# Optimization experiments

Hardware: AMD Instinct MI355X
Metric: run time of the kernel (lower is better)

Reference implementation:

```python
import jax, jax.numpy as jnp
import numpy as np

N0, E0 = 20000, 100000
N1, E1 = 100000, 400000
N2, E2 = 400000, 800000
D = 128
LN_EPS = 1e-5


def gconv(h, src, dst, n, W, b):
    """DGL GraphConv, norm='both', on graph (src,dst) with self-loops added."""
    loops = jnp.arange(n, dtype=src.dtype)
    s = jnp.concatenate([src, loops])
    d = jnp.concatenate([dst, loops])
    ones = jnp.ones(s.shape[0], h.dtype)
    deg_out = jax.ops.segment_sum(ones, s, num_segments=n)
    deg_in = jax.ops.segment_sum(ones, d, num_segments=n)
    hn = (h * jax.lax.rsqrt(jnp.maximum(deg_out, 1.0))[:, None]) @ W
    agg = jax.ops.segment_sum(hn[s], d, num_segments=n)
    return agg * jax.lax.rsqrt(jnp.maximum(deg_in, 1.0))[:, None] + b


def lgcore(src, dst, n, curr_h, fus_inputs, p):
    """fus_inputs: list of (fusion_input [n,D] (already inc-matmul'd), scale [D])."""
    convW, convb, fusW, fusb, catW, catb, convw, lng, lnb = p
    cs = gconv(curr_h, src, dst, n, convW, convb) * convw[None, :]
    res = jnp.concatenate([jax.nn.relu(cs), cs], axis=1)
    for fin, sw in fus_inputs:
        fs = gconv(fin, src, dst, n, fusW, fusb) * sw[None, :]
        res = res + jnp.concatenate([jax.nn.relu(fs), fs], axis=1)
    out = res @ catW + catb
    mu = jnp.mean(out, axis=-1, keepdims=True)
    var = jnp.var(out, axis=-1, keepdims=True)
    return (out - mu) * jax.lax.rsqrt(var + LN_EPS) * lng + lnb


def lgnn(h0, h1, h2, src0, dst0, src1, dst1, src2, dst2,
         convW, convb, fusW, fusb, catW, catb, convw, tdw, buw, lng, lnb):
    def params(i):
        return (convW[i], convb[i], fusW[i], fusb[i], catW[i], catb[i], convw[i], lng[i], lnb[i])
    # level 0: top_down core (idx 0). inc0 @ h1 -> segment_sum of h1 over dst0
    td0 = jax.ops.segment_sum(h1, dst0, num_segments=N0)
    out0 = lgcore(src0, dst0, N0, h0, [(td0, tdw[0])], params(0))
    # level 1: 'both' core (idx 2). inc0^T @ h0 -> gather; inc1 @ h2 -> segment_sum
    bu1 = h0[dst0]                                   # [E0=N1, D]
    td1 = jax.ops.segment_sum(h2, dst1, num_segments=N1)
    out1 = lgcore(src1, dst1, N1, h1, [(bu1, buw[2]), (td1, tdw[2])], params(2))
    # level 2: bottom_up core (idx 1). inc1^T @ h1 -> gather
    bu2 = h1[dst1]                                   # [E1=N2, D]
    out2 = lgcore(src2, dst2, N2, h2, [(bu2, buw[1])], params(1))
    return out0, out1, out2


def setup_inputs() -> dict:
    key = jax.random.key(0)
    ks = jax.random.split(key, 16)
    sc = 1.0 / np.sqrt(D)
    return {
        "h0": jax.random.normal(ks[0], (N0, D), jnp.float32),
        "h1": jax.random.normal(ks[1], (N1, D), jnp.float32),
        "h2": jax.random.normal(ks[2], (N2, D), jnp.float32),
        "src0": jax.random.randint(ks[3], (E0,), 0, N0, jnp.int32),
        "dst0": jax.random.randint(ks[4], (E0,), 0, N0, jnp.int32),
        "src1": jax.random.randint(ks[5], (E1,), 0, N1, jnp.int32),
        "dst1": jax.random.randint(ks[6], (E1,), 0, N1, jnp.int32),
        "src2": jax.random.randint(ks[7], (E2,), 0, N2, jnp.int32),
        "dst2": jax.random.randint(ks[8], (E2,), 0, N2, jnp.int32),
        "convW": jax.random.normal(ks[9], (3, D, D), jnp.float32) * sc,
        "convb": jnp.zeros((3, D), jnp.float32),
        "fusW": jax.random.normal(ks[10], (3, D, D), jnp.float32) * sc,
        "fusb": jnp.zeros((3, D), jnp.float32),
        "catW": jax.random.normal(ks[11], (3, 2 * D, D), jnp.float32) * (1.0 / np.sqrt(2 * D)),
        "catb": jnp.zeros((3, D), jnp.float32),
        "convw": jax.random.uniform(ks[12], (3, D), jnp.float32),
        "tdw": jax.random.uniform(ks[13], (3, D), jnp.float32),
        "buw": jax.random.uniform(ks[14], (3, D), jnp.float32),
        "lng": jnp.ones((3, D), jnp.float32),
        "lnb": jnp.zeros((3, D), jnp.float32),
    }


def reference(h0, h1, h2, src0, dst0, src1, dst1, src2, dst2,
              convW, convb, fusW, fusb, catW, catb, convw, tdw, buw, lng, lnb):
    return lgnn(h0, h1, h2, src0, dst0, src1, dst1, src2, dst2,
                convW, convb, fusW, fusb, catW, catb, convw, tdw, buw, lng, lnb)
```

## Files before the change

### kernel.cpp

```cpp
#include <hip/hip_runtime.h>

#define D 128
#define LN_EPS 1e-5f

static constexpr int cN0 = 20000,  cE0 = 100000;
static constexpr int cN1 = 100000, cE1 = 400000;
static constexpr int cN2 = 400000, cE2 = 800000;

typedef _Float16 f16;
typedef _Float16 f16x8 __attribute__((ext_vector_type(8)));
typedef float f32x4 __attribute__((ext_vector_type(4)));
typedef unsigned short u16x8 __attribute__((ext_vector_type(8)));

__device__ inline float h2f(unsigned short u) {
    return (float)__builtin_bit_cast(_Float16, u);
}
__device__ inline unsigned short f2h(float f) {
    return __builtin_bit_cast(unsigned short, (_Float16)f);
}
__device__ inline float4 h4_to_f4(ushort4 v) {
    return make_float4(h2f(v.x), h2f(v.y), h2f(v.z), h2f(v.w));
}


__global__ void k_count(const int* __restrict__ src, const int* __restrict__ dst,
                        int* cnt_out, int* cnt_in, int E) {
    int e = blockIdx.x * blockDim.x + threadIdx.x;
    if (e < E) {
        atomicAdd(&cnt_out[src[e]], 1);
        atomicAdd(&cnt_in[dst[e]], 1);
    }
}

__global__ void k_bsum(const int* __restrict__ cnt, int* bsum, int n) {
    __shared__ int sd[256];
    int t = threadIdx.x;
    int base = blockIdx.x * 1024 + t * 4;
    int s = 0;
#pragma unroll
    for (int i = 0; i < 4; ++i) { int idx = base + i; if (idx < n) s += cnt[idx]; }
    sd[t] = s; __syncthreads();
    for (int off = 128; off > 0; off >>= 1) {
        if (t < off) sd[t] += sd[t + off];
        __syncthreads();
    }
    if (t == 0) bsum[blockIdx.x] = sd[0];
}

__global__ void k_scan_write(const int* __restrict__ cnt, const int* __restrict__ bsum,
                             int* __restrict__ ptr, int n, int E) {
    __shared__ int sd[256];
    __shared__ int so[256];
    int t = threadIdx.x, blk = blockIdx.x;
    int off = 0;
    for (int i = t; i < blk; i += 256) off += bsum[i];
    so[t] = off; __syncthreads();
    for (int o = 128; o > 0; o >>= 1) { if (t < o) so[t] += so[t + o]; __syncthreads(); }
    int boff = so[0];
    int base = blk * 1024 + t * 4;
    int vals[4]; int s = 0;
#pragma unroll
    for (int i = 0; i < 4; ++i) { int idx = base + i; vals[i] = (idx < n) ? cnt[idx] : 0; s += vals[i]; }
    sd[t] = s; __syncthreads();
    for (int o = 1; o < 256; o <<= 1) {
        int x = (t >= o) ? sd[t - o] : 0;
        __syncthreads();
        sd[t] += x;
        __syncthreads();
    }
    int run = boff + sd[t] - s;
#pragma unroll
    for (int i = 0; i < 4; ++i) {
        int idx = base + i;
        if (idx < n) ptr[idx] = run;
        run += vals[i];
    }
    if (blk == 0 && t == 0) ptr[n] = E;
}

__global__ void k_rin_cursor(const int* __restrict__ cnt_out, const int* __restrict__ cnt_in,
                             const int* __restrict__ ptr, float* __restrict__ rout,
                             float* __restrict__ rin, int* __restrict__ cursor, int n) {
    int i = blockIdx.x * blockDim.x + threadIdx.x;
    if (i < n) {
        rout[i] = rsqrtf((float)(cnt_out[i] + 1));
        rin[i]  = rsqrtf((float)(cnt_in[i] + 1));
        cursor[i] = ptr[i];
    }
}

__global__ void k_fill(const int* __restrict__ src, const int* __restrict__ dst,
                       int* cursor, int* __restrict__ eid, int* __restrict__ srcs, int E) {
    int e = blockIdx.x * blockDim.x + threadIdx.x;
    if (e < E) {
        int p = atomicAdd(&cursor[dst[e]], 1);
        eid[p] = e;
        srcs[p] = src[e];
    }
}

__global__ void k_segsum_rows(float* __restrict__ X, const int* __restrict__ ptr,
                              const int* __restrict__ eid, const float* __restrict__ table,
                              int n) {
    int wid = (blockIdx.x * blockDim.x + threadIdx.x) >> 6;
    int lane = threadIdx.x & 63;
    if (wid >= n) return;
    int j = lane * 2;
    float2 acc = make_float2(0.f, 0.f);
    int p0 = ptr[wid], p1 = ptr[wid + 1];
    for (int p = p0; p < p1; ++p) {
        int e = eid[p];
        const float2 x = *(const float2*)(table + (size_t)e * D + j);
        acc.x += x.x; acc.y += x.y;
    }
    *(float2*)(X + (size_t)wid * D + j) = acc;
}

__global__ void k_prep_w(const float* __restrict__ convW, const float* __restrict__ fusW,
                         const float* __restrict__ catW,
                         unsigned short* __restrict__ cWt, unsigned short* __restrict__ fWt,
                         unsigned short* __restrict__ kWt) {
    int t = blockIdx.x * 256 + threadIdx.x;
    if (t < 98304) {
        int mi = t / 16384, r = t % 16384;
        const float* W = (mi < 3) ? (convW + mi * 16384) : (fusW + (mi - 3) * 16384);
        unsigned short* T = (mi < 3) ? (cWt + mi * 16384) : (fWt + (mi - 3) * 16384);
        int n = r >> 7, k = r & 127;
        T[r] = f2h(W[k * 128 + n]);
    } else if (t < 196608) {
        int t2 = t - 98304;
        int mi = t2 / 32768, r = t2 % 32768;
        int n = r >> 8, k = r & 255;
        kWt[mi * 32768 + r] = f2h(catW[mi * 32768 + k * 128 + n]);
    }
}

template<bool GATHER>
__global__ __launch_bounds__(256) void k_gconv_mfma(
        const float* __restrict__ A, const int* __restrict__ ridx,
        const float* __restrict__ rs, const unsigned short* __restrict__ Wt,
        unsigned short* __restrict__ C, int M) {
    __shared__ __align__(16) unsigned short Ws[128 * 128];
    int tid = threadIdx.x;
#pragma unroll
    for (int i = 0; i < 8; ++i) {
        int lb = (tid + i * 256) << 4;
        int n = lb >> 8;
        int sw = lb ^ ((n & 7) << 4);
        *(u16x8*)((char*)Ws + sw) = *(const u16x8*)((const char*)Wt + lb);
    }
    __syncthreads();
    int w = tid >> 6, l = tid & 63;
    int g = l >> 4, ln = l & 15;
    int row0 = blockIdx.x * 128 + w * 32;
    int m0 = row0 + ln, m1 = m0 + 16;
    bool v0 = m0 < M, v1 = m1 < M;
    int sr0 = m0, sr1 = m1;
    if (GATHER) {
        sr0 = v0 ? ridx[m0] : 0;
        sr1 = v1 ? ridx[m1] : 0;
    }
    const float* a0p = A + (size_t)sr0 * 128;
    const float* a1p = A + (size_t)sr1 * 128;
    f32x4 acc[2][8] = {};
#pragma unroll
    for (int k0 = 0; k0 < 128; k0 += 32) {
        int kk = k0 + g * 8;
        f16x8 b0 = {}, b1 = {};
        if (v0) {
            float4 x = *(const float4*)(a0p + kk);
            float4 y = *(const float4*)(a0p + kk + 4);
            b0[0] = (f16)x.x; b0[1] = (f16)x.y; b0[2] = (f16)x.z; b0[3] = (f16)x.w;
            b0[4] = (f16)y.x; b0[5] = (f16)y.y; b0[6] = (f16)y.z; b0[7] = (f16)y.w;
        }
        if (v1) {
            float4 x = *(const float4*)(a1p + kk);
            float4 y = *(const float4*)(a1p + kk + 4);
            b1[0] = (f16)x.x; b1[1] = (f16)x.y; b1[2] = (f16)x.z; b1[3] = (f16)x.w;
            b1[4] = (f16)y.x; b1[5] = (f16)y.y; b1[6] = (f16)y.z; b1[7] = (f16)y.w;
        }
#pragma unroll
        for (int nf = 0; nf < 8; ++nf) {
            int n = nf * 16 + ln;
            int sw = (n * 256 + kk * 2) ^ ((n & 7) << 4);
            f16x8 a = *(const f16x8*)((const char*)Ws + sw);
            acc[0][nf] = __builtin_amdgcn_mfma_f32_16x16x32_f16(a, b0, acc[0][nf], 0, 0, 0);
            acc[1][nf] = __builtin_amdgcn_mfma_f32_16x16x32_f16(a, b1, acc[1][nf], 0, 0, 0);
        }
    }
    float s0 = v0 ? rs[m0] : 0.f;
    float s1 = v1 ? rs[m1] : 0.f;
#pragma unroll
    for (int mf = 0; mf < 2; ++mf) {
        int m = mf ? m1 : m0;
        if (m >= M) continue;
        float s = mf ? s1 : s0;
        unsigned short* cp = C + (size_t)m * 128 + g * 4;
#pragma unroll
        for (int nf = 0; nf < 8; ++nf) {
            f32x4 v = acc[mf][nf];
            ushort4 o;
            o.x = f2h(v[0] * s); o.y = f2h(v[1] * s);
            o.z = f2h(v[2] * s); o.w = f2h(v[3] * s);
            *(ushort4*)(cp + nf * 16) = o;
        }
    }
}

template<int NT>
__global__ void k_agg_multi(const unsigned short* __restrict__ H0,
                            const unsigned short* __restrict__ H1,
                            const unsigned short* __restrict__ H2,
                            const int* __restrict__ ptr, const int* __restrict__ srcs,
                            const float* __restrict__ rin,
                            const float* __restrict__ b0, const float* __restrict__ b1,
                            const float* __restrict__ b2,
                            const float* __restrict__ c0, const float* __restrict__ c1,
                            const float* __restrict__ c2,
                            unsigned short* __restrict__ RES, int n) {
    int node = (blockIdx.x * blockDim.x + threadIdx.x) >> 5;
    int lane = threadIdx.x & 31;
    if (node >= n) return;
    int j = lane * 4;

    float4 a0 = make_float4(0.f, 0.f, 0.f, 0.f), a1 = a0, a2 = a0;
    a0 = h4_to_f4(*(const ushort4*)(H0 + (size_t)node * D + j));
    if (NT > 1) a1 = h4_to_f4(*(const ushort4*)(H1 + (size_t)node * D + j));
    if (NT > 2) a2 = h4_to_f4(*(const ushort4*)(H2 + (size_t)node * D + j));

    int p0 = ptr[node], p1 = ptr[node + 1];
    for (int p = p0; p < p1; ++p) {
        int s = srcs[p];
        float4 x0 = h4_to_f4(*(const ushort4*)(H0 + (size_t)s * D + j));
        a0.x += x0.x; a0.y += x0.y; a0.z += x0.z; a0.w += x0.w;
        if (NT > 1) {
            float4 x1 = h4_to_f4(*(const ushort4*)(H1 + (size_t)s * D + j));
            a1.x += x1.x; a1.y += x1.y; a1.z += x1.z; a1.w += x1.w;
        }
        if (NT > 2) {
            float4 x2 = h4_to_f4(*(const ushort4*)(H2 + (size_t)s * D + j));
            a2.x += x2.x; a2.y += x2.y; a2.z += x2.z; a2.w += x2.w;
        }
    }

    float ri = rin[node];
    float4 bb0 = *(const float4*)(b0 + j);
    float4 cc0 = *(const float4*)(c0 + j);
    float4 v, rsum, ssum;
    v.x = (a0.x * ri + bb0.x) * cc0.x;
    v.y = (a0.y * ri + bb0.y) * cc0.y;
    v.z = (a0.z * ri + bb0.z) * cc0.z;
    v.w = (a0.w * ri + bb0.w) * cc0.w;
    rsum = make_float4(fmaxf(v.x, 0.f), fmaxf(v.y, 0.f), fmaxf(v.z, 0.f), fmaxf(v.w, 0.f));
    ssum = v;
    if (NT > 1) {
        float4 bb = *(const float4*)(b1 + j);
        float4 cc = *(const float4*)(c1 + j);
        v.x = (a1.x * ri + bb.x) * cc.x;
        v.y = (a1.y * ri + bb.y) * cc.y;
        v.z = (a1.z * ri + bb.z) * cc.z;
        v.w = (a1.w * ri + bb.w) * cc.w;
        rsum.x += fmaxf(v.x, 0.f); rsum.y += fmaxf(v.y, 0.f);
        rsum.z += fmaxf(v.z, 0.f); rsum.w += fmaxf(v.w, 0.f);
        ssum.x += v.x; ssum.y += v.y; ssum.z += v.z; ssum.w += v.w;
    }
    if (NT > 2) {
        float4 bb = *(const float4*)(b2 + j);
        float4 cc = *(const float4*)(c2 + j);
        v.x = (a2.x * ri + bb.x) * cc.x;
        v.y = (a2.y * ri + bb.y) * cc.y;
        v.z = (a2.z * ri + bb.z) * cc.z;
        v.w = (a2.w * ri + bb.w) * cc.w;
        rsum.x += fmaxf(v.x, 0.f); rsum.y += fmaxf(v.y, 0.f);
        rsum.z += fmaxf(v.z, 0.f); rsum.w += fmaxf(v.w, 0.f);
        ssum.x += v.x; ssum.y += v.y; ssum.z += v.z; ssum.w += v.w;
    }
    unsigned short* r = RES + (size_t)node * (2 * D) + j;
    ushort4 o1, o2;
    o1.x = f2h(rsum.x); o1.y = f2h(rsum.y); o1.z = f2h(rsum.z); o1.w = f2h(rsum.w);
    o2.x = f2h(ssum.x); o2.y = f2h(ssum.y); o2.z = f2h(ssum.z); o2.w = f2h(ssum.w);
    *(ushort4*)r = o1;
    *(ushort4*)(r + D) = o2;
}

__global__ __launch_bounds__(256) void k_cat_ln_mfma(
        const unsigned short* __restrict__ RESh, const unsigned short* __restrict__ Wt,
        const float* __restrict__ bias, const float* __restrict__ gam,
        const float* __restrict__ bet, float* __restrict__ out, int M) {
    __shared__ __align__(16) unsigned short Ws[128 * 256];
    int tid = threadIdx.x;
#pragma unroll
    for (int i = 0; i < 16; ++i) {
        int lb = (tid + i * 256) << 4;
        int n = lb >> 9;
        int sw = lb ^ ((n & 7) << 4);
        *(u16x8*)((char*)Ws + sw) = *(const u16x8*)((const char*)Wt + lb);
    }
    __syncthreads();
    int w = tid >> 6, l = tid & 63;
    int g = l >> 4, ln = l & 15;
    int row0 = blockIdx.x * 128 + w * 32;
    int m0 = row0 + ln, m1 = m0 + 16;
    bool v0 = m0 < M, v1 = m1 < M;
    const unsigned short* r0p = RESh + (size_t)m0 * 256;
    const unsigned short* r1p = RESh + (size_t)m1 * 256;
    f32x4 acc[2][8] = {};
#pragma unroll
    for (int k0 = 0; k0 < 256; k0 += 32) {
        int kk = k0 + g * 8;
        f16x8 b0 = {}, b1 = {};
        if (v0) b0 = *(const f16x8*)(r0p + kk);
        if (v1) b1 = *(const f16x8*)(r1p + kk);
#pragma unroll
        for (int nf = 0; nf < 8; ++nf) {
            int n = nf * 16 + ln;
            int sw = (n * 512 + kk * 2) ^ ((n & 7) << 4);
            f16x8 a = *(const f16x8*)((const char*)Ws + sw);
            acc[0][nf] = __builtin_amdgcn_mfma_f32_16x16x32_f16(a, b0, acc[0][nf], 0, 0, 0);
            acc[1][nf] = __builtin_amdgcn_mfma_f32_16x16x32_f16(a, b1, acc[1][nf], 0, 0, 0);
        }
    }
#pragma unroll
    for (int mf = 0; mf < 2; ++mf) {
        float x[8][4];
        float s = 0.f, ss = 0.f;
#pragma unroll
        for (int nf = 0; nf < 8; ++nf) {
            float4 b = *(const float4*)(bias + nf * 16 + g * 4);
            f32x4 v = acc[mf][nf];
            x[nf][0] = v[0] + b.x; x[nf][1] = v[1] + b.y;
            x[nf][2] = v[2] + b.z; x[nf][3] = v[3] + b.w;
            s += x[nf][0] + x[nf][1] + x[nf][2] + x[nf][3];
            ss += x[nf][0] * x[nf][0] + x[nf][1] * x[nf][1]
                + x[nf][2] * x[nf][2] + x[nf][3] * x[nf][3];
        }
        s  += __shfl_xor(s, 16, 64);  s  += __shfl_xor(s, 32, 64);
        ss += __shfl_xor(ss, 16, 64); ss += __shfl_xor(ss, 32, 64);
        float mu = s * (1.0f / 128.0f);
        float var = ss * (1.0f / 128.0f) - mu * mu;
        float inv = rsqrtf(var + LN_EPS);
        int m = mf ? m1 : m0;
        if (m < M) {
            float* op = out + (size_t)m * 128 + g * 4;
#pragma unroll
            for (int nf = 0; nf < 8; ++nf) {
                float4 gv = *(const float4*)(gam + nf * 16 + g * 4);
                float4 ev = *(const float4*)(bet + nf * 16 + g * 4);
                float4 o;
                o.x = (x[nf][0] - mu) * inv * gv.x + ev.x;
                o.y = (x[nf][1] - mu) * inv * gv.y + ev.y;
                o.z = (x[nf][2] - mu) * inv * gv.z + ev.z;
                o.w = (x[nf][3] - mu) * inv * gv.w + ev.w;
                *(float4*)(op + nf * 16) = o;
            }
        }
    }
}

__global__ void k_ws_too_small(float* out) {
    if (threadIdx.x == 0 && blockIdx.x == 0) out[0] = 12345678.f;
}


struct Lvl {
    int n, E;
    const int *src, *dst;
    int *cnt_out, *cnt_in, *ptr, *cursor, *eid, *srcs;
    float *rout, *rin;
};

static inline char* bump(char*& p, size_t bytes, void** out) {
    *out = (void*)p;
    p += (bytes + 255) & ~(size_t)255;
    return p;
}

extern "C" void kernel_launch(void* const* d_in, const int* in_sizes, int n_in,
                              void* d_out, int out_size, void* d_ws, size_t ws_size,
                              hipStream_t stream) {
    const float* h0 = (const float*)d_in[0];
    const float* h1 = (const float*)d_in[1];
    const float* h2 = (const float*)d_in[2];
    const int* src0 = (const int*)d_in[3];
    const int* dst0 = (const int*)d_in[4];
    const int* src1 = (const int*)d_in[5];
    const int* dst1 = (const int*)d_in[6];
    const int* src2 = (const int*)d_in[7];
    const int* dst2 = (const int*)d_in[8];
    const float* convW = (const float*)d_in[9];
    const float* convb = (const float*)d_in[10];
    const float* fusW  = (const float*)d_in[11];
    const float* fusb  = (const float*)d_in[12];
    const float* catW  = (const float*)d_in[13];
    const float* catb  = (const float*)d_in[14];
    const float* convw = (const float*)d_in[15];
    const float* tdw   = (const float*)d_in[16];
    const float* buw   = (const float*)d_in[17];
    const float* lng   = (const float*)d_in[18];
    const float* lnb   = (const float*)d_in[19];
    float* out = (float*)d_out;

    char* p = (char*)d_ws;
    void *vX, *vHNa, *vHNb, *vHNc, *vRES, *vbsum, *vcWt, *vfWt, *vkWt;
    bump(p, (size_t)cN1 * D * 4, &vX);
    bump(p, (size_t)cN2 * D * 2, &vHNa);
    bump(p, (size_t)cN2 * D * 2, &vHNb);
    bump(p, (size_t)cN1 * D * 2, &vHNc);
    bump(p, (size_t)cN2 * 2 * D * 2, &vRES);
    bump(p, 512 * 4, &vbsum);
    bump(p, (size_t)3 * 128 * 128 * 2, &vcWt);
    bump(p, (size_t)3 * 128 * 128 * 2, &vfWt);
    bump(p, (size_t)3 * 128 * 256 * 2, &vkWt);
    float* X = (float*)vX;
    unsigned short* HNa = (unsigned short*)vHNa;
    unsigned short* HNb = (unsigned short*)vHNb;
    unsigned short* HNc = (unsigned short*)vHNc;
    unsigned short* RESh = (unsigned short*)vRES;
    int* bsum = (int*)vbsum;
    unsigned short* cWt = (unsigned short*)vcWt;
    unsigned short* fWt = (unsigned short*)vfWt;
    unsigned short* kWt = (unsigned short*)vkWt;

    Lvl lv[3];
    lv[0] = {cN0, cE0, src0, dst0};
    lv[1] = {cN1, cE1, src1, dst1};
    lv[2] = {cN2, cE2, src2, dst2};
    for (int L = 0; L < 3; ++L) {
        Lvl& v = lv[L];
        void* t;
        bump(p, (size_t)v.n * 4, &t);       v.cnt_out = (int*)t;
        bump(p, (size_t)v.n * 4, &t);       v.cnt_in  = (int*)t;
        bump(p, (size_t)(v.n + 1) * 4, &t); v.ptr     = (int*)t;
        bump(p, (size_t)v.n * 4, &t);       v.cursor  = (int*)t;
        bump(p, (size_t)v.E * 4, &t);       v.eid     = (int*)t;
        bump(p, (size_t)v.E * 4, &t);       v.srcs    = (int*)t;
        bump(p, (size_t)v.n * 4, &t);       v.rout    = (float*)t;
        bump(p, (size_t)v.n * 4, &t);       v.rin     = (float*)t;
    }
    size_t need = (size_t)(p - (char*)d_ws);
    if (need > ws_size) {
        hipLaunchKernelGGL(k_ws_too_small, dim3(1), dim3(64), 0, stream, out);
        return;
    }

    k_prep_w<<<768, 256, 0, stream>>>(convW, fusW, catW, cWt, fWt, kWt);

    for (int L = 0; L < 3; ++L) {
        Lvl& v = lv[L];
        hipMemsetAsync(v.cnt_out, 0, (size_t)v.n * 4, stream);
        hipMemsetAsync(v.cnt_in, 0, (size_t)v.n * 4, stream);
        k_count<<<(v.E + 255) / 256, 256, 0, stream>>>(v.src, v.dst, v.cnt_out, v.cnt_in, v.E);
        int nb = (v.n + 1023) / 1024;
        k_bsum<<<nb, 256, 0, stream>>>(v.cnt_in, bsum, v.n);
        k_scan_write<<<nb, 256, 0, stream>>>(v.cnt_in, bsum, v.ptr, v.n, v.E);
        k_rin_cursor<<<(v.n + 255) / 256, 256, 0, stream>>>(v.cnt_out, v.cnt_in, v.ptr,
                                                            v.rout, v.rin, v.cursor, v.n);
        k_fill<<<(v.E + 255) / 256, 256, 0, stream>>>(v.src, v.dst, v.cursor, v.eid, v.srcs, v.E);
    }

    auto gemm = [&](int L, const float* A, const int* ridx, const unsigned short* Wt,
                    unsigned short* HN) {
        Lvl& v = lv[L];
        int nb = (v.n + 127) / 128;
        if (ridx)
            k_gconv_mfma<true><<<nb, 256, 0, stream>>>(A, ridx, v.rout, Wt, HN, v.n);
        else
            k_gconv_mfma<false><<<nb, 256, 0, stream>>>(A, nullptr, v.rout, Wt, HN, v.n);
    };

    {
        Lvl& v = lv[0];
        gemm(0, h0, nullptr, cWt, HNa);
        k_segsum_rows<<<(cN0 + 3) / 4, 256, 0, stream>>>(X, v.ptr, v.eid, h1, cN0);
        gemm(0, X, nullptr, fWt, HNb);
        k_agg_multi<2><<<(cN0 * 32 + 255) / 256, 256, 0, stream>>>(
            HNa, HNb, HNa, v.ptr, v.srcs, v.rin,
            convb + 0, fusb + 0, convb + 0,
            convw + 0, tdw + 0, convw + 0, RESh, cN0);
        k_cat_ln_mfma<<<(cN0 + 127) / 128, 256, 0, stream>>>(RESh, kWt, catb + 0,
                                                             lng + 0, lnb + 0, out, cN0);
    }

    {
        Lvl& v = lv[1];
        const int o1 = 2 * D;
        gemm(1, h1, nullptr, cWt + 2 * 16384, HNa);
        gemm(1, h0, dst0, fWt + 2 * 16384, HNb);
        k_segsum_rows<<<(cN1 + 3) / 4, 256, 0, stream>>>(X, v.ptr, v.eid, h2, cN1);
        gemm(1, X, nullptr, fWt + 2 * 16384, HNc);
        k_agg_multi<3><<<(cN1 * 32 + 255) / 256, 256, 0, stream>>>(
            HNa, HNb, HNc, v.ptr, v.srcs, v.rin,
            convb + o1, fusb + o1, fusb + o1,
            convw + o1, buw + o1, tdw + o1, RESh, cN1);
        k_cat_ln_mfma<<<(cN1 + 127) / 128, 256, 0, stream>>>(RESh, kWt + 2 * 32768, catb + o1,
                                                             lng + o1, lnb + o1,
                                                             out + (size_t)cN0 * D, cN1);
    }

    {
        Lvl& v = lv[2];
        const int o1 = 1 * D;
        gemm(2, h2, nullptr, cWt + 1 * 16384, HNa);
        gemm(2, h1, dst1, fWt + 1 * 16384, HNb);
        k_agg_multi<2><<<(cN2 * 32 + 255) / 256, 256, 0, stream>>>(
            HNa, HNb, HNa, v.ptr, v.srcs, v.rin,
            convb + o1, fusb + o1, convb + o1,
            convw + o1, buw + o1, convw + o1, RESh, cN2);
        k_cat_ln_mfma<<<(cN2 + 127) / 128, 256, 0, stream>>>(RESh, kWt + 1 * 32768, catb + o1,
                                                             lng + o1, lnb + o1,
                                                             out + (size_t)(cN0 + cN1) * D, cN2);
    }
}
```

Before: 1.334 ms.

## Aggregate before projecting and fuse per-source GEMMs with concat-LN

Reorders each graph convolution as aggregate-then-multiply, using linearity of the weight matmul. It gathers fp16 inputs (converted once up front) scaled by out-degree, then runs a single fused kernel that does all per-source 128x128 MFMA GEMMs, applies bias and scale, relu and sum, the concat GEMM and the LayerNorm. This removes the HN intermediate buffers and the RES round trip through global memory, and folds the per-feature scales into the weights. The cost is that weights are read from global/L1 inside the MFMA loop rather than staged in LDS, and inputs plus segment sums are now held in fp16, which adds rounding error.

```diff
diff --git a/kernel.cpp b/kernel.cpp
--- a/kernel.cpp
+++ b/kernel.cpp
@@ -17,9 +17,6 @@
 }
 __device__ inline unsigned short f2h(float f) {
     return __builtin_bit_cast(unsigned short, (_Float16)f);
-}
-__device__ inline float4 h4_to_f4(ushort4 v) {
-    return make_float4(h2f(v.x), h2f(v.y), h2f(v.z), h2f(v.w));
 }
 
 
@@ -99,260 +96,272 @@
     }
 }
 
-__global__ void k_segsum_rows(float* __restrict__ X, const int* __restrict__ ptr,
-                              const int* __restrict__ eid, const float* __restrict__ table,
-                              int n) {
+__global__ void k_f2h(const float* __restrict__ in, unsigned short* __restrict__ o, int n4) {
+    int i = blockIdx.x * 256 + threadIdx.x;
+    if (i < n4) {
+        float4 v = ((const float4*)in)[i];
+        ushort4 u;
+        u.x = f2h(v.x); u.y = f2h(v.y); u.z = f2h(v.z); u.w = f2h(v.w);
+        ((ushort4*)o)[i] = u;
+    }
+}
+
+__global__ void k_segsum_h(unsigned short* __restrict__ X, const int* __restrict__ ptr,
+                           const int* __restrict__ eid, const unsigned short* __restrict__ table,
+                           int n) {
     int wid = (blockIdx.x * blockDim.x + threadIdx.x) >> 6;
     int lane = threadIdx.x & 63;
     if (wid >= n) return;
     int j = lane * 2;
-    float2 acc = make_float2(0.f, 0.f);
+    float ax = 0.f, ay = 0.f;
     int p0 = ptr[wid], p1 = ptr[wid + 1];
     for (int p = p0; p < p1; ++p) {
         int e = eid[p];
-        const float2 x = *(const float2*)(table + (size_t)e * D + j);
-        acc.x += x.x; acc.y += x.y;
-    }
-    *(float2*)(X + (size_t)wid * D + j) = acc;
+        ushort2 u = *(const ushort2*)(table + (size_t)e * D + j);
+        ax += h2f(u.x); ay += h2f(u.y);
+    }
+    ushort2 o; o.x = f2h(ax); o.y = f2h(ay);
+    *(ushort2*)(X + (size_t)wid * D + j) = o;
 }
 
 __global__ void k_prep_w(const float* __restrict__ convW, const float* __restrict__ fusW,
                          const float* __restrict__ catW,
-                         unsigned short* __restrict__ cWt, unsigned short* __restrict__ fWt,
-                         unsigned short* __restrict__ kWt) {
+                         const float* __restrict__ convw, const float* __restrict__ tdw,
+                         const float* __restrict__ buw,
+                         unsigned short* __restrict__ sWt, unsigned short* __restrict__ kWt) {
     int t = blockIdx.x * 256 + threadIdx.x;
-    if (t < 98304) {
-        int mi = t / 16384, r = t % 16384;
-        const float* W = (mi < 3) ? (convW + mi * 16384) : (fusW + (mi - 3) * 16384);
-        unsigned short* T = (mi < 3) ? (cWt + mi * 16384) : (fWt + (mi - 3) * 16384);
+    if (t < 7 * 16384) {
+        int slot = t / 16384, r = t % 16384;
         int n = r >> 7, k = r & 127;
-        T[r] = f2h(W[k * 128 + n]);
-    } else if (t < 196608) {
-        int t2 = t - 98304;
-        int mi = t2 / 32768, r = t2 % 32768;
-        int n = r >> 8, k = r & 255;
-        kWt[mi * 32768 + r] = f2h(catW[mi * 32768 + k * 128 + n]);
-    }
-}
-
-template<bool GATHER>
-__global__ __launch_bounds__(256) void k_gconv_mfma(
-        const float* __restrict__ A, const int* __restrict__ ridx,
-        const float* __restrict__ rs, const unsigned short* __restrict__ Wt,
-        unsigned short* __restrict__ C, int M) {
-    __shared__ __align__(16) unsigned short Ws[128 * 128];
-    int tid = threadIdx.x;
-#pragma unroll
-    for (int i = 0; i < 8; ++i) {
-        int lb = (tid + i * 256) << 4;
-        int n = lb >> 8;
-        int sw = lb ^ ((n & 7) << 4);
-        *(u16x8*)((char*)Ws + sw) = *(const u16x8*)((const char*)Wt + lb);
-    }
-    __syncthreads();
-    int w = tid >> 6, l = tid & 63;
-    int g = l >> 4, ln = l & 15;
-    int row0 = blockIdx.x * 128 + w * 32;
-    int m0 = row0 + ln, m1 = m0 + 16;
-    bool v0 = m0 < M, v1 = m1 < M;
-    int sr0 = m0, sr1 = m1;
-    if (GATHER) {
-        sr0 = v0 ? ridx[m0] : 0;
-        sr1 = v1 ? ridx[m1] : 0;
-    }
-    const float* a0p = A + (size_t)sr0 * 128;
-    const float* a1p = A + (size_t)sr1 * 128;
-    f32x4 acc[2][8] = {};
-#pragma unroll
-    for (int k0 = 0; k0 < 128; k0 += 32) {
-        int kk = k0 + g * 8;
-        f16x8 b0 = {}, b1 = {};
-        if (v0) {
-            float4 x = *(const float4*)(a0p + kk);
-            float4 y = *(const float4*)(a0p + kk + 4);
-            b0[0] = (f16)x.x; b0[1] = (f16)x.y; b0[2] = (f16)x.z; b0[3] = (f16)x.w;
-            b0[4] = (f16)y.x; b0[5] = (f16)y.y; b0[6] = (f16)y.z; b0[7] = (f16)y.w;
-        }
-        if (v1) {
-            float4 x = *(const float4*)(a1p + kk);
-            float4 y = *(const float4*)(a1p + kk + 4);
-            b1[0] = (f16)x.x; b1[1] = (f16)x.y; b1[2] = (f16)x.z; b1[3] = (f16)x.w;
-            b1[4] = (f16)y.x; b1[5] = (f16)y.y; b1[6] = (f16)y.z; b1[7] = (f16)y.w;
-        }
-#pragma unroll
-        for (int nf = 0; nf < 8; ++nf) {
-            int n = nf * 16 + ln;
-            int sw = (n * 256 + kk * 2) ^ ((n & 7) << 4);
-            f16x8 a = *(const f16x8*)((const char*)Ws + sw);
-            acc[0][nf] = __builtin_amdgcn_mfma_f32_16x16x32_f16(a, b0, acc[0][nf], 0, 0, 0);
-            acc[1][nf] = __builtin_amdgcn_mfma_f32_16x16x32_f16(a, b1, acc[1][nf], 0, 0, 0);
-        }
-    }
-    float s0 = v0 ? rs[m0] : 0.f;
-    float s1 = v1 ? rs[m1] : 0.f;
-#pragma unroll
-    for (int mf = 0; mf < 2; ++mf) {
-        int m = mf ? m1 : m0;
-        if (m >= M) continue;
-        float s = mf ? s1 : s0;
-        unsigned short* cp = C + (size_t)m * 128 + g * 4;
-#pragma unroll
-        for (int nf = 0; nf < 8; ++nf) {
-            f32x4 v = acc[mf][nf];
-            ushort4 o;
-            o.x = f2h(v[0] * s); o.y = f2h(v[1] * s);
-            o.z = f2h(v[2] * s); o.w = f2h(v[3] * s);
-            *(ushort4*)(cp + nf * 16) = o;
-        }
-    }
-}
-
-template<int NT>
-__global__ void k_agg_multi(const unsigned short* __restrict__ H0,
-                            const unsigned short* __restrict__ H1,
-                            const unsigned short* __restrict__ H2,
-                            const int* __restrict__ ptr, const int* __restrict__ srcs,
-                            const float* __restrict__ rin,
-                            const float* __restrict__ b0, const float* __restrict__ b1,
-                            const float* __restrict__ b2,
-                            const float* __restrict__ c0, const float* __restrict__ c1,
-                            const float* __restrict__ c2,
-                            unsigned short* __restrict__ RES, int n) {
+        const float* W; const float* cw;
+        switch (slot) {
+            case 0: W = convW;              cw = convw;            break;
+            case 1: W = fusW;               cw = tdw;              break;
+            case 2: W = convW + 2 * 16384;  cw = convw + 2 * 128;  break;
+            case 3: W = fusW + 2 * 16384;   cw = buw + 2 * 128;    break;
+            case 4: W = fusW + 2 * 16384;   cw = tdw + 2 * 128;    break;
+            case 5: W = convW + 1 * 16384;  cw = convw + 1 * 128;  break;
+            default: W = fusW + 1 * 16384;  cw = buw + 1 * 128;    break;
+        }
+        sWt[t] = f2h(W[k * 128 + n] * cw[n]);
+    } else {
+        int t2 = t - 7 * 16384;
+        if (t2 < 3 * 32768) {
+            int mi = t2 / 32768, r = t2 % 32768;
+            int n = r >> 8, k = r & 255;
+            kWt[mi * 32768 + r] = f2h(catW[mi * 32768 + k * 128 + n]);
+        }
+    }
+}
+
+template<int NT, bool G1>
+__global__ void k_aggh(const unsigned short* __restrict__ F0,
+                       const unsigned short* __restrict__ F1,
+                       const unsigned short* __restrict__ F2,
+                       const int* __restrict__ gidx,
+                       const float* __restrict__ rout,
+                       const int* __restrict__ ptr, const int* __restrict__ srcs,
+                       unsigned short* __restrict__ A0, unsigned short* __restrict__ A1,
+                       unsigned short* __restrict__ A2, int n) {
     int node = (blockIdx.x * blockDim.x + threadIdx.x) >> 5;
     int lane = threadIdx.x & 31;
     if (node >= n) return;
     int j = lane * 4;
 
-    float4 a0 = make_float4(0.f, 0.f, 0.f, 0.f), a1 = a0, a2 = a0;
-    a0 = h4_to_f4(*(const ushort4*)(H0 + (size_t)node * D + j));
-    if (NT > 1) a1 = h4_to_f4(*(const ushort4*)(H1 + (size_t)node * D + j));
-    if (NT > 2) a2 = h4_to_f4(*(const ushort4*)(H2 + (size_t)node * D + j));
+    float rt = rout[node];
+    float4 a0, a1, a2;
+    {
+        ushort4 u = *(const ushort4*)(F0 + (size_t)node * D + j);
+        a0 = make_float4(h2f(u.x) * rt, h2f(u.y) * rt, h2f(u.z) * rt, h2f(u.w) * rt);
+    }
+    if (NT > 1) {
+        int i1 = G1 ? gidx[node] : node;
+        ushort4 u = *(const ushort4*)(F1 + (size_t)i1 * D + j);
+        a1 = make_float4(h2f(u.x) * rt, h2f(u.y) * rt, h2f(u.z) * rt, h2f(u.w) * rt);
+    }
+    if (NT > 2) {
+        ushort4 u = *(const ushort4*)(F2 + (size_t)node * D + j);
+        a2 = make_float4(h2f(u.x) * rt, h2f(u.y) * rt, h2f(u.z) * rt, h2f(u.w) * rt);
+    }
 
     int p0 = ptr[node], p1 = ptr[node + 1];
-    for (int p = p0; p < p1; ++p) {
-        int s = srcs[p];
-        float4 x0 = h4_to_f4(*(const ushort4*)(H0 + (size_t)s * D + j));
-        a0.x += x0.x; a0.y += x0.y; a0.z += x0.z; a0.w += x0.w;
+    int p = p0;
+    for (; p + 2 <= p1; p += 2) {
+        int sA = srcs[p], sB = srcs[p + 1];
+        float rA = rout[sA], rB = rout[sB];
+        ushort4 uA = *(const ushort4*)(F0 + (size_t)sA * D + j);
+        ushort4 uB = *(const ushort4*)(F0 + (size_t)sB * D + j);
+        a0.x += h2f(uA.x) * rA + h2f(uB.x) * rB;
+        a0.y += h2f(uA.y) * rA + h2f(uB.y) * rB;
+        a0.z += h2f(uA.z) * rA + h2f(uB.z) * rB;
+        a0.w += h2f(uA.w) * rA + h2f(uB.w) * rB;
         if (NT > 1) {
-            float4 x1 = h4_to_f4(*(const ushort4*)(H1 + (size_t)s * D + j));
-            a1.x += x1.x; a1.y += x1.y; a1.z += x1.z; a1.w += x1.w;
+            int iA = G1 ? gidx[sA] : sA;
+            int iB = G1 ? gidx[sB] : sB;
+            ushort4 vA = *(const ushort4*)(F1 + (size_t)iA * D + j);
+            ushort4 vB = *(const ushort4*)(F1 + (size_t)iB * D + j);
+            a1.x += h2f(vA.x) * rA + h2f(vB.x) * rB;
+            a1.y += h2f(vA.y) * rA + h2f(vB.y) * rB;
+            a1.z += h2f(vA.z) * rA + h2f(vB.z) * rB;
+            a1.w += h2f(vA.w) * rA + h2f(vB.w) * rB;
         }
         if (NT > 2) {
-            float4 x2 = h4_to_f4(*(const ushort4*)(H2 + (size_t)s * D + j));
-            a2.x += x2.x; a2.y += x2.y; a2.z += x2.z; a2.w += x2.w;
-        }
-    }
-
-    float ri = rin[node];
-    float4 bb0 = *(const float4*)(b0 + j);
-    float4 cc0 = *(const float4*)(c0 + j);
-    float4 v, rsum, ssum;
-    v.x = (a0.x * ri + bb0.x) * cc0.x;
-    v.y = (a0.y * ri + bb0.y) * cc0.y;
-    v.z = (a0.z * ri + bb0.z) * cc0.z;
-    v.w = (a0.w * ri + bb0.w) * cc0.w;
-    rsum = make_float4(fmaxf(v.x, 0.f), fmaxf(v.y, 0.f), fmaxf(v.z, 0.f), fmaxf(v.w, 0.f));
-    ssum = v;
+            ushort4 vA = *(const ushort4*)(F2 + (size_t)sA * D + j);
+            ushort4 vB = *(const ushort4*)(F2 + (size_t)sB * D + j);
+            a2.x += h2f(vA.x) * rA + h2f(vB.x) * rB;
+            a2.y += h2f(vA.y) * rA + h2f(vB.y) * rB;
+            a2.z += h2f(vA.z) * rA + h2f(vB.z) * rB;
+            a2.w += h2f(vA.w) * rA + h2f(vB.w) * rB;
+        }
+    }
+    if (p < p1) {
+        int sA = srcs[p];
+        float rA = rout[sA];
+        ushort4 uA = *(const ushort4*)(F0 + (size_t)sA * D + j);
+        a0.x += h2f(uA.x) * rA; a0.y += h2f(uA.y) * rA;
+        a0.z += h2f(uA.z) * rA; a0.w += h2f(uA.w) * rA;
+        if (NT > 1) {
+            int iA = G1 ? gidx[sA] : sA;
+            ushort4 vA = *(const ushort4*)(F1 + (size_t)iA * D + j);
+            a1.x += h2f(vA.x) * rA; a1.y += h2f(vA.y) * rA;
+            a1.z += h2f(vA.z) * rA; a1.w += h2f(vA.w) * rA;
+        }
+        if (NT > 2) {
+            ushort4 vA = *(const ushort4*)(F2 + (size_t)sA * D + j);
+            a2.x += h2f(vA.x) * rA; a2.y += h2f(vA.y) * rA;
+            a2.z += h2f(vA.z) * rA; a2.w += h2f(vA.w) * rA;
+        }
+    }
+
+    ushort4 o;
+    o.x = f2h(a0.x); o.y = f2h(a0.y); o.z = f2h(a0.z); o.w = f2h(a0.w);
+    *(ushort4*)(A0 + (size_t)node * D + j) = o;
     if (NT > 1) {
-        float4 bb = *(const float4*)(b1 + j);
-        float4 cc = *(const float4*)(c1 + j);
-        v.x = (a1.x * ri + bb.x) * cc.x;
-        v.y = (a1.y * ri + bb.y) * cc.y;
-        v.z = (a1.z * ri + bb.z) * cc.z;
-        v.w = (a1.w * ri + bb.w) * cc.w;
-        rsum.x += fmaxf(v.x, 0.f); rsum.y += fmaxf(v.y, 0.f);
-        rsum.z += fmaxf(v.z, 0.f); rsum.w += fmaxf(v.w, 0.f);
-        ssum.x += v.x; ssum.y += v.y; ssum.z += v.z; ssum.w += v.w;
+        o.x = f2h(a1.x); o.y = f2h(a1.y); o.z = f2h(a1.z); o.w = f2h(a1.w);
+        *(ushort4*)(A1 + (size_t)node * D + j) = o;
     }
     if (NT > 2) {
-        float4 bb = *(const float4*)(b2 + j);
-        float4 cc = *(const float4*)(c2 + j);
-        v.x = (a2.x * ri + bb.x) * cc.x;
-        v.y = (a2.y * ri + bb.y) * cc.y;
-        v.z = (a2.z * ri + bb.z) * cc.z;
-        v.w = (a2.w * ri + bb.w) * cc.w;
-        rsum.x += fmaxf(v.x, 0.f); rsum.y += fmaxf(v.y, 0.f);
-        rsum.z += fmaxf(v.z, 0.f); rsum.w += fmaxf(v.w, 0.f);
-        ssum.x += v.x; ssum.y += v.y; ssum.z += v.z; ssum.w += v.w;
-    }
-    unsigned short* r = RES + (size_t)node * (2 * D) + j;
-    ushort4 o1, o2;
-    o1.x = f2h(rsum.x); o1.y = f2h(rsum.y); o1.z = f2h(rsum.z); o1.w = f2h(rsum.w);
-    o2.x = f2h(ssum.x); o2.y = f2h(ssum.y); o2.z = f2h(ssum.z); o2.w = f2h(ssum.w);
-    *(ushort4*)r = o1;
-    *(ushort4*)(r + D) = o2;
-}
-
-__global__ __launch_bounds__(256) void k_cat_ln_mfma(
-        const unsigned short* __restrict__ RESh, const unsigned short* __restrict__ Wt,
-        const float* __restrict__ bias, const float* __restrict__ gam,
-        const float* __restrict__ bet, float* __restrict__ out, int M) {
-    __shared__ __align__(16) unsigned short Ws[128 * 256];
+        o.x = f2h(a2.x); o.y = f2h(a2.y); o.z = f2h(a2.z); o.w = f2h(a2.w);
+        *(ushort4*)(A2 + (size_t)node * D + j) = o;
+    }
+}
+
+template<int NT>
+__global__ __launch_bounds__(256) void k_mega(
+        const unsigned short* __restrict__ A0h, const unsigned short* __restrict__ A1h,
+        const unsigned short* __restrict__ A2h,
+        const unsigned short* __restrict__ W0, const unsigned short* __restrict__ W1,
+        const unsigned short* __restrict__ W2,
+        const float* __restrict__ pb0, const float* __restrict__ pc0,
+        const float* __restrict__ pb1, const float* __restrict__ pc1,
+        const float* __restrict__ pb2, const float* __restrict__ pc2,
+        const float* __restrict__ rin,
+        const unsigned short* __restrict__ kWt,
+        const float* __restrict__ cbias, const float* __restrict__ gam,
+        const float* __restrict__ bet,
+        float* __restrict__ out, int M) {
+    __shared__ __align__(16) unsigned short tile[64 * 256];
     int tid = threadIdx.x;
-#pragma unroll
-    for (int i = 0; i < 16; ++i) {
-        int lb = (tid + i * 256) << 4;
-        int n = lb >> 9;
-        int sw = lb ^ ((n & 7) << 4);
-        *(u16x8*)((char*)Ws + sw) = *(const u16x8*)((const char*)Wt + lb);
+    int w = tid >> 6, l = tid & 63, g = l >> 4, ln = l & 15;
+    int mloc = w * 16 + ln;
+    int m = blockIdx.x * 64 + mloc;
+    bool vm = m < M;
+    float ri = vm ? rin[m] : 0.f;
+
+    f32x4 rr[8] = {};
+    f32x4 sv[8] = {};
+
+    const unsigned short* Ah[3] = {A0h, A1h, A2h};
+    const unsigned short* Wh[3] = {W0, W1, W2};
+    const float* pbs[3] = {pb0, pb1, pb2};
+    const float* pcs[3] = {pc0, pc1, pc2};
+
+#pragma unroll
+    for (int t = 0; t < NT; ++t) {
+        f32x4 acc[8] = {};
+        const unsigned short* ap = Ah[t] + (size_t)m * 128;
+#pragma unroll
+        for (int k0 = 0; k0 < 128; k0 += 32) {
+            int kk = k0 + g * 8;
+            f16x8 bf = {};
+            if (vm) bf = *(const f16x8*)(ap + kk);
+#pragma unroll
+            for (int nf = 0; nf < 8; ++nf) {
+                f16x8 af = *(const f16x8*)(Wh[t] + (size_t)(nf * 16 + ln) * 128 + kk);
+                acc[nf] = __builtin_amdgcn_mfma_f32_16x16x32_f16(af, bf, acc[nf], 0, 0, 0);
+            }
+        }
+#pragma unroll
+        for (int nf = 0; nf < 8; ++nf) {
+            float4 bb = *(const float4*)(pbs[t] + nf * 16 + g * 4);
+            float4 cc = *(const float4*)(pcs[t] + nf * 16 + g * 4);
+            f32x4 a = acc[nf];
+            float v0 = ri * a[0] + bb.x * cc.x;
+            float v1 = ri * a[1] + bb.y * cc.y;
+            float v2 = ri * a[2] + bb.z * cc.z;
+            float v3 = ri * a[3] + bb.w * cc.w;
+            rr[nf][0] += fmaxf(v0, 0.f); rr[nf][1] += fmaxf(v1, 0.f);
+            rr[nf][2] += fmaxf(v2, 0.f); rr[nf][3] += fmaxf(v3, 0.f);
+            sv[nf][0] += v0; sv[nf][1] += v1; sv[nf][2] += v2; sv[nf][3] += v3;
+        }
+    }
+
+#pragma unroll
+    for (int nf = 0; nf < 8; ++nf) {
+        int n = nf * 16 + g * 4;
+        int byr = (mloc * 512 + n * 2) ^ ((mloc & 7) << 4);
+        ushort4 ur, us;
+        ur.x = f2h(rr[nf][0]); ur.y = f2h(rr[nf][1]);
+        ur.z = f2h(rr[nf][2]); ur.w = f2h(rr[nf][3]);
+        us.x = f2h(sv[nf][0]); us.y = f2h(sv[nf][1]);
+        us.z = f2h(sv[nf][2]); us.w = f2h(sv[nf][3]);
+        *(ushort4*)((char*)tile + byr) = ur;
+        *(ushort4*)((char*)tile + byr + 256) = us;
     }
     __syncthreads();
-    int w = tid >> 6, l = tid & 63;
-    int g = l >> 4, ln = l & 15;
-    int row0 = blockIdx.x * 128 + w * 32;
-    int m0 = row0 + ln, m1 = m0 + 16;
-    bool v0 = m0 < M, v1 = m1 < M;
-    const unsigned short* r0p = RESh + (size_t)m0 * 256;
-    const unsigned short* r1p = RESh + (size_t)m1 * 256;
-    f32x4 acc[2][8] = {};
+
+    f32x4 acc2[8] = {};
 #pragma unroll
     for (int k0 = 0; k0 < 256; k0 += 32) {
         int kk = k0 + g * 8;
-        f16x8 b0 = {}, b1 = {};
-        if (v0) b0 = *(const f16x8*)(r0p + kk);
-        if (v1) b1 = *(const f16x8*)(r1p + kk);
+        int by = (mloc * 512 + kk * 2) ^ ((mloc & 7) << 4);
+        f16x8 bf = *(const f16x8*)((const char*)tile + by);
 #pragma unroll
         for (int nf = 0; nf < 8; ++nf) {
-            int n = nf * 16 + ln;
-            int sw = (n * 512 + kk * 2) ^ ((n & 7) << 4);
-            f16x8 a = *(const f16x8*)((const char*)Ws + sw);
-            acc[0][nf] = __builtin_amdgcn_mfma_f32_16x16x32_f16(a, b0, acc[0][nf], 0, 0, 0);
-            acc[1][nf] = __builtin_amdgcn_mfma_f32_16x16x32_f16(a, b1, acc[1][nf], 0, 0, 0);
-        }
-    }
-#pragma unroll
-    for (int mf = 0; mf < 2; ++mf) {
-        float x[8][4];
-        float s = 0.f, ss = 0.f;
+            f16x8 af = *(const f16x8*)(kWt + (size_t)(nf * 16 + ln) * 256 + kk);
+            acc2[nf] = __builtin_amdgcn_mfma_f32_16x16x32_f16(af, bf, acc2[nf], 0, 0, 0);
+        }
+    }
+
+    float x[8][4];
+    float sum = 0.f, ssum = 0.f;
+#pragma unroll
+    for (int nf = 0; nf < 8; ++nf) {
+        float4 b = *(const float4*)(cbias + nf * 16 + g * 4);
+        f32x4 vv = acc2[nf];
+        x[nf][0] = vv[0] + b.x; x[nf][1] = vv[1] + b.y;
+        x[nf][2] = vv[2] + b.z; x[nf][3] = vv[3] + b.w;
+        sum += x[nf][0] + x[nf][1] + x[nf][2] + x[nf][3];
+        ssum += x[nf][0] * x[nf][0] + x[nf][1] * x[nf][1]
+              + x[nf][2] * x[nf][2] + x[nf][3] * x[nf][3];
+    }
+    sum  += __shfl_xor(sum, 16, 64);  sum  += __shfl_xor(sum, 32, 64);
+    ssum += __shfl_xor(ssum, 16, 64); ssum += __shfl_xor(ssum, 32, 64);
+    float mu = sum * (1.0f / 128.0f);
+    float var = ssum * (1.0f / 128.0f) - mu * mu;
+    float inv = rsqrtf(var + LN_EPS);
+    if (vm) {
+        float* op = out + (size_t)m * 128 + g * 4;
 #pragma unroll
         for (int nf = 0; nf < 8; ++nf) {
-            float4 b = *(const float4*)(bias + nf * 16 + g * 4);
-            f32x4 v = acc[mf][nf];
-            x[nf][0] = v[0] + b.x; x[nf][1] = v[1] + b.y;
-            x[nf][2] = v[2] + b.z; x[nf][3] = v[3] + b.w;
-            s += x[nf][0] + x[nf][1] + x[nf][2] + x[nf][3];
-            ss += x[nf][0] * x[nf][0] + x[nf][1] * x[nf][1]
-                + x[nf][2] * x[nf][2] + x[nf][3] * x[nf][3];
-        }
-        s  += __shfl_xor(s, 16, 64);  s  += __shfl_xor(s, 32, 64);
-        ss += __shfl_xor(ss, 16, 64); ss += __shfl_xor(ss, 32, 64);
-        float mu = s * (1.0f / 128.0f);
-        float var = ss * (1.0f / 128.0f) - mu * mu;
-        float inv = rsqrtf(var + LN_EPS);
-        int m = mf ? m1 : m0;
-        if (m < M) {
-            float* op = out + (size_t)m * 128 + g * 4;
-#pragma unroll
-            for (int nf = 0; nf < 8; ++nf) {
-                float4 gv = *(const float4*)(gam + nf * 16 + g * 4);
-                float4 ev = *(const float4*)(bet + nf * 16 + g * 4);
-                float4 o;
-                o.x = (x[nf][0] - mu) * inv * gv.x + ev.x;
-                o.y = (x[nf][1] - mu) * inv * gv.y + ev.y;
-                o.z = (x[nf][2] - mu) * inv * gv.z + ev.z;
-                o.w = (x[nf][3] - mu) * inv * gv.w + ev.w;
-                *(float4*)(op + nf * 16) = o;
-            }
+            float4 gv = *(const float4*)(gam + nf * 16 + g * 4);
+            float4 ev = *(const float4*)(bet + nf * 16 + g * 4);
+            float4 o;
+            o.x = (x[nf][0] - mu) * inv * gv.x + ev.x;
+            o.y = (x[nf][1] - mu) * inv * gv.y + ev.y;
+            o.z = (x[nf][2] - mu) * inv * gv.z + ev.z;
+            o.w = (x[nf][3] - mu) * inv * gv.w + ev.w;
+            *(float4*)(op + nf * 16) = o;
         }
     }
 }
@@ -401,25 +410,27 @@
     float* out = (float*)d_out;
 
     char* p = (char*)d_ws;
-    void *vX, *vHNa, *vHNb, *vHNc, *vRES, *vbsum, *vcWt, *vfWt, *vkWt;
-    bump(p, (size_t)cN1 * D * 4, &vX);
-    bump(p, (size_t)cN2 * D * 2, &vHNa);
-    bump(p, (size_t)cN2 * D * 2, &vHNb);
-    bump(p, (size_t)cN1 * D * 2, &vHNc);
-    bump(p, (size_t)cN2 * 2 * D * 2, &vRES);
+    void *vh0f, *vh1f, *vh2f, *vXf, *vAa, *vAb, *vAc, *vsWt, *vkWt, *vbsum;
+    bump(p, (size_t)cN0 * D * 2, &vh0f);
+    bump(p, (size_t)cN1 * D * 2, &vh1f);
+    bump(p, (size_t)cN2 * D * 2, &vh2f);
+    bump(p, (size_t)cN1 * D * 2, &vXf);
+    bump(p, (size_t)cN2 * D * 2, &vAa);
+    bump(p, (size_t)cN2 * D * 2, &vAb);
+    bump(p, (size_t)cN1 * D * 2, &vAc);
+    bump(p, (size_t)7 * 16384 * 2, &vsWt);
+    bump(p, (size_t)3 * 32768 * 2, &vkWt);
     bump(p, 512 * 4, &vbsum);
-    bump(p, (size_t)3 * 128 * 128 * 2, &vcWt);
-    bump(p, (size_t)3 * 128 * 128 * 2, &vfWt);
-    bump(p, (size_t)3 * 128 * 256 * 2, &vkWt);
-    float* X = (float*)vX;
-    unsigned short* HNa = (unsigned short*)vHNa;
-    unsigned short* HNb = (unsigned short*)vHNb;
-    unsigned short* HNc = (unsigned short*)vHNc;
-    unsigned short* RESh = (unsigned short*)vRES;
+    unsigned short* h0f = (unsigned short*)vh0f;
+    unsigned short* h1f = (unsigned short*)vh1f;
+    unsigned short* h2f = (unsigned short*)vh2f;
+    unsigned short* Xf  = (unsigned short*)vXf;
+    unsigned short* Aa  = (unsigned short*)vAa;
+    unsigned short* Ab  = (unsigned short*)vAb;
+    unsigned short* Ac  = (unsigned short*)vAc;
+    unsigned short* sWt = (unsigned short*)vsWt;
+    unsigned short* kWt = (unsigned short*)vkWt;
     int* bsum = (int*)vbsum;
-    unsigned short* cWt = (unsigned short*)vcWt;
-    unsigned short* fWt = (unsigned short*)vfWt;
-    unsigned short* kWt = (unsigned short*)vkWt;
 
     Lvl lv[3];
     lv[0] = {cN0, cE0, src0, dst0};
@@ -443,7 +454,10 @@
         return;
     }
 
-    k_prep_w<<<768, 256, 0, stream>>>(convW, fusW, catW, cWt, fWt, kWt);
+    k_prep_w<<<832, 256, 0, stream>>>(convW, fusW, catW, convw, tdw, buw, sWt, kWt);
+    k_f2h<<<(cN0 * D / 4 + 255) / 256, 256, 0, stream>>>(h0, h0f, cN0 * D / 4);
+    k_f2h<<<(cN1 * D / 4 + 255) / 256, 256, 0, stream>>>(h1, h1f, cN1 * D / 4);
+    k_f2h<<<(cN2 * D / 4 + 255) / 256, 256, 0, stream>>>(h2, h2f, cN2 * D / 4);
 
     for (int L = 0; L < 3; ++L) {
         Lvl& v = lv[L];
@@ -458,56 +472,42 @@
         k_fill<<<(v.E + 255) / 256, 256, 0, stream>>>(v.src, v.dst, v.cursor, v.eid, v.srcs, v.E);
     }
 
-    auto gemm = [&](int L, const float* A, const int* ridx, const unsigned short* Wt,
-                    unsigned short* HN) {
-        Lvl& v = lv[L];
-        int nb = (v.n + 127) / 128;
-        if (ridx)
-            k_gconv_mfma<true><<<nb, 256, 0, stream>>>(A, ridx, v.rout, Wt, HN, v.n);
-        else
-            k_gconv_mfma<false><<<nb, 256, 0, stream>>>(A, nullptr, v.rout, Wt, HN, v.n);
-    };
-
     {
         Lvl& v = lv[0];
-        gemm(0, h0, nullptr, cWt, HNa);
-        k_segsum_rows<<<(cN0 + 3) / 4, 256, 0, stream>>>(X, v.ptr, v.eid, h1, cN0);
-        gemm(0, X, nullptr, fWt, HNb);
-        k_agg_multi<2><<<(cN0 * 32 + 255) / 256, 256, 0, stream>>>(
-            HNa, HNb, HNa, v.ptr, v.srcs, v.rin,
-            convb + 0, fusb + 0, convb + 0,
-            convw + 0, tdw + 0, convw + 0, RESh, cN0);
-        k_cat_ln_mfma<<<(cN0 + 127) / 128, 256, 0, stream>>>(RESh, kWt, catb + 0,
-                                                             lng + 0, lnb + 0, out, cN0);
+        k_segsum_h<<<(cN0 + 3) / 4, 256, 0, stream>>>(Xf, v.ptr, v.eid, h1f, cN0);
+        k_aggh<2, false><<<(cN0 * 32 + 255) / 256, 256, 0, stream>>>(
+            h0f, Xf, Xf, nullptr, v.rout, v.ptr, v.srcs, Aa, Ab, Ab, cN0);
+        k_mega<2><<<(cN0 + 63) / 64, 256, 0, stream>>>(
+            Aa, Ab, Ab,
+            sWt + 0 * 16384, sWt + 1 * 16384, sWt,
+            convb, convw, fusb, tdw, convb, convw,
+            v.rin, kWt, catb, lng, lnb, out, cN0);
     }
 
     {
         Lvl& v = lv[1];
         const int o1 = 2 * D;
-        gemm(1, h1, nullptr, cWt + 2 * 16384, HNa);
-        gemm(1, h0, dst0, fWt + 2 * 16384, HNb);
-        k_segsum_rows<<<(cN1 + 3) / 4, 256, 0, stream>>>(X, v.ptr, v.eid, h2, cN1);
-        gemm(1, X, nullptr, fWt + 2 * 16384, HNc);
-        k_agg_multi<3><<<(cN1 * 32 + 255) / 256, 256, 0, stream>>>(
-            HNa, HNb, HNc, v.ptr, v.srcs, v.rin,
-            convb + o1, fusb + o1, fusb + o1,
-            convw + o1, buw + o1, tdw + o1, RESh, cN1);
-        k_cat_ln_mfma<<<(cN1 + 127) / 128, 256, 0, stream>>>(RESh, kWt + 2 * 32768, catb + o1,
-                                                             lng + o1, lnb + o1,
-                                                             out + (size_t)cN0 * D, cN1);
+        k_segsum_h<<<(cN1 + 3) / 4, 256, 0, stream>>>(Xf, v.ptr, v.eid, h2f, cN1);
+        k_aggh<3, true><<<(cN1 * 32 + 255) / 256, 256, 0, stream>>>(
+            h1f, h0f, Xf, dst0, v.rout, v.ptr, v.srcs, Aa, Ab, Ac, cN1);
+        k_mega<3><<<(cN1 + 63) / 64, 256, 0, stream>>>(
+            Aa, Ab, Ac,
+            sWt + 2 * 16384, sWt + 3 * 16384, sWt + 4 * 16384,
+            convb + o1, convw + o1, fusb + o1, buw + o1, fusb + o1, tdw + o1,
+            v.rin, kWt + 2 * 32768, catb + o1, lng + o1, lnb + o1,
+            out + (size_t)cN0 * D, cN1);
     }
 
     {
         Lvl& v = lv[2];
         const int o1 = 1 * D;
-        gemm(2, h2, nullptr, cWt + 1 * 16384, HNa);
-        gemm(2, h1, dst1, fWt + 1 * 16384, HNb);
-        k_agg_multi<2><<<(cN2 * 32 + 255) / 256, 256, 0, stream>>>(
-            HNa, HNb, HNa, v.ptr, v.srcs, v.rin,
-            convb + o1, fusb + o1, convb + o1,
-            convw + o1, buw + o1, convw + o1, RESh, cN2);
-        k_cat_ln_mfma<<<(cN2 + 127) / 128, 256, 0, stream>>>(RESh, kWt + 1 * 32768, catb + o1,
-                                                             lng + o1, lnb + o1,
-                                                             out + (size_t)(cN0 + cN1) * D, cN2);
-    }
-}
+        k_aggh<2, true><<<(cN2 * 32 + 255) / 256, 256, 0, stream>>>(
+            h2f, h1f, h1f, dst1, v.rout, v.ptr, v.srcs, Aa, Ab, Ab, cN2);
+        k_mega<2><<<(cN2 + 63) / 64, 256, 0, stream>>>(
+            Aa, Ab, Ab,
+            sWt + 5 * 16384, sWt + 6 * 16384, sWt,
+            convb + o1, convw + o1, fusb + o1, buw + o1, convb + o1, convw + o1,
+            v.rin, kWt + 1 * 32768, catb + o1, lng + o1, lnb + o1,
+            out + (size_t)(cN0 + cN1) * D, cN2);
+    }
+}
```

After: 1.658 ms. 24.3% more time.
